# Kernel optimization log

Hardware: AMD Instinct MI355X
Metric: run time of the kernel (lower is better)

The kernel has to match this reference:

```python
import jax, jax.numpy as jnp
import numpy as np

N_ARY = 2
H = 128
X_SIZE = 128
DEPTH = 18  # levels in complete binary tree; n = 2^DEPTH - 1 = 262143 nodes


def setup_inputs() -> dict:
    key = jax.random.key(0)
    k0, k1, k2, k3 = jax.random.split(key, 4)
    n = (N_ARY ** DEPTH - 1) // (N_ARY - 1)
    x = jax.random.normal(k0, (n, X_SIZE), jnp.float32)
    W_w = jax.random.normal(k1, (2 * H, X_SIZE), jnp.float32) * 0.05
    W_b = jnp.zeros((2 * H,), jnp.float32)
    U_f = jax.random.normal(k2, (H, N_ARY * H), jnp.float32) * 0.05
    U_hc = jax.random.normal(k3, (H, N_ARY * H), jnp.float32) * 0.05
    return {"x": x, "W_w": W_w, "W_b": W_b, "U_f": U_f, "U_hc": U_hc, "depth": DEPTH}


def reference(x, W_w, W_b, U_f, U_hc, depth):
    """Tree-structured single-forget-gate MGU on a complete N_ARY tree.

    Node i (level-order) has children N_ARY*i+1 .. N_ARY*i+N_ARY. Levels are
    processed bottom-up (leaves first), matching DGL topological prop_nodes.
    """
    n_ary, h_size = N_ARY, H
    n = x.shape[0]
    wx = x @ W_w.T + W_b                      # [n, 2h]
    w_hc_x = wx[:, :h_size]                   # candidate pre-activation part
    w_f_x = wx[:, h_size:]                    # forget-gate pre-activation part
    h = jnp.zeros((n, h_size), x.dtype)
    for lvl in range(depth - 1, -1, -1):
        start = (n_ary ** lvl - 1) // (n_ary - 1)
        size = n_ary ** lvl
        whc = w_hc_x[start:start + size]
        wf = w_f_x[start:start + size]
        if lvl == depth - 1:
            # leaves: mailbox empty -> f_in = 0, h_cat = 0, h_sum = 0
            f = jax.nn.sigmoid(wf)
            new_h = (1.0 - f) * jnp.tanh(whc)
        else:
            # children of [start, start+size) occupy the contiguous next-level block
            child_start = n_ary * start + 1
            h_child = h[child_start:child_start + size * n_ary]
            h_child = h_child.reshape(size, n_ary, h_size)
            h_cat = h_child.reshape(size, n_ary * h_size)
            f = jax.nn.sigmoid(h_cat @ U_f.T + wf)
            f_rep = jnp.tile(f, (1, n_ary))
            h_cand = jnp.tanh(whc + (f_rep * h_cat) @ U_hc.T)
            new_h = f * h_child.sum(axis=1) + (1.0 - f) * h_cand
        h = h.at[start:start + size].set(new_h)
    return h
```

## Files before the change

kernel.cpp:

```cpp
#include <hip/hip_runtime.h>
#include <cmath>

#define NT 256

#define NTOT   262143
#define NINT   131071

#define WHC_OFF   0
#define WF_OFF    (NINT * 128)
#define UFT_OFF   (2 * NINT * 128)
#define UHCT_OFF  (UFT_OFF + 32768)
#define PKWW_OFF  (UHCT_OFF + 32768)
#define PKUF_OFF  (PKWW_OFF + 98304)
#define PKUHC_OFF (PKUF_OFF + 98304)
#define WS_FLOATS (PKUHC_OFF + 98304)
#define WS_BYTES  ((size_t)WS_FLOATS * 4)

#define PA_PACK 0x120100
#define PB_PACK 0x102010

typedef __attribute__((ext_vector_type(8))) short short8v;
typedef __attribute__((ext_vector_type(4))) float f32x4;

__device__ __forceinline__ float sigmoid_(float v) {
    return 1.0f / (1.0f + expf(-v));
}

__device__ __forceinline__ void split3(float a, unsigned &t0, unsigned &t1, unsigned &t2) {
    unsigned u0 = __float_as_uint(a) & 0xffff0000u;
    float f0 = __uint_as_float(u0);
    float r1 = a - f0;
    unsigned u1 = __float_as_uint(r1) & 0xffff0000u;
    float f1 = __uint_as_float(u1);
    float r2 = r1 - f1;
    unsigned u2 = __float_as_uint(r2) & 0xffff0000u;
    t0 = u0 >> 16; t1 = u1 >> 16; t2 = u2 >> 16;
}

__global__ __launch_bounds__(NT) void prep_pack(
    const float* __restrict__ Ww, const float* __restrict__ Uf,
    const float* __restrict__ Uhc, float* __restrict__ ws)
{
    int t = blockIdx.x * NT + threadIdx.x;
    if (t < 32768) { int k = t >> 7, j = t & 127; ws[UFT_OFF + t] = Uf[j * 256 + k]; return; }
    t -= 32768;
    if (t < 32768) { int k = t >> 7, j = t & 127; ws[UHCT_OFF + t] = Uhc[j * 256 + k]; return; }
    t -= 32768;

    const float* src; int term; uint4* dst; int q;
    if (t < 24576) {
        q = t;
        int l = q & 63, j = (q >> 6) & 15, s = q >> 10;
        int p = s >> 2, ks = s & 3;
        term = (PB_PACK >> (p * 4)) & 3;
        int kb = ks * 32 + (l >> 4) * 8, col = j * 16 + (l & 15);
        src = Ww + col * 128 + kb;
        dst = (uint4*)(ws + PKWW_OFF);
    } else if (t < 49152) {
        q = t - 24576;
        int l = q & 63, j = (q >> 6) & 7, s = q >> 9;
        int p = s >> 3, ks = s & 7;
        term = (PB_PACK >> (p * 4)) & 3;
        int kb = ks * 32 + (l >> 4) * 8, col = j * 16 + (l & 15);
        src = Uf + col * 256 + kb;
        dst = (uint4*)(ws + PKUF_OFF);
    } else if (t < 73728) {
        q = t - 49152;
        int l = q & 63, j = (q >> 6) & 7, s = q >> 9;
        int p = s >> 3, ks = s & 7;
        term = (PB_PACK >> (p * 4)) & 3;
        int kb = ks * 32 + (l >> 4) * 8, col = j * 16 + (l & 15);
        src = Uhc + col * 256 + kb;
        dst = (uint4*)(ws + PKUHC_OFF);
    } else return;

    unsigned hv[8];
#pragma unroll
    for (int e = 0; e < 8; ++e) {
        unsigned a, b, c; split3(src[e], a, b, c);
        hv[e] = (term == 0) ? a : (term == 1 ? b : c);
    }
    uint4 o;
    o.x = hv[0] | (hv[1] << 16); o.y = hv[2] | (hv[3] << 16);
    o.z = hv[4] | (hv[5] << 16); o.w = hv[6] | (hv[7] << 16);
    dst[q] = o;
}

#define LOADC(srcbase) { const uint4* s_ = (srcbase); \
    nx0 = s_[tid]; nx1 = s_[tid + 512]; nx2 = s_[tid + 1024]; nx3 = s_[tid + 1536]; }
#define WRITEC(dstbase) { uint4* d_ = (dstbase); \
    d_[tid] = nx0; d_[tid + 512] = nx1; d_[tid + 1024] = nx2; d_[tid + 1536] = nx3; }

__global__ __launch_bounds__(512) void wx_mfma4(
    const float* __restrict__ x, const float* __restrict__ ws_all,
    const float* __restrict__ Wb, float* __restrict__ ws, float* __restrict__ h)
{
    __shared__ short As[128 * 384];
    __shared__ uint4 sBb[2][2048];
    char* Asb = (char*)As;
    const int tid = threadIdx.x;
    const int nbase = blockIdx.x * 128;
    const uint4* pkb = (const uint4*)(ws_all + PKWW_OFF);

    uint4 nx0, nx1, nx2, nx3;
    LOADC(pkb);

    for (int i = 0; i < 8; ++i) {
        int idx = i * 512 + tid;
        int m = idx >> 5, g = idx & 31;
        int node = nbase + m; if (node > NTOT - 1) node = NTOT - 1;
        float4 v = *(const float4*)(x + (size_t)node * 128 + g * 4);
        unsigned a0[4], a1[4], a2[4];
        split3(v.x, a0[0], a1[0], a2[0]); split3(v.y, a0[1], a1[1], a2[1]);
        split3(v.z, a0[2], a1[2], a2[2]); split3(v.w, a0[3], a1[3], a2[3]);
        int ks = g >> 3, kg = (g >> 1) & 3, hw = (g & 1) * 8;
        int kss = ks ^ ((m >> 2) & 3), kgs = kg ^ (m & 3);
        char* base = Asb + m * 768 + kgs * 16 + hw;
        *(uint2*)(base + ((0 * 4 + kss) << 6)) = make_uint2(a0[0] | (a0[1] << 16), a0[2] | (a0[3] << 16));
        *(uint2*)(base + ((1 * 4 + kss) << 6)) = make_uint2(a1[0] | (a1[1] << 16), a1[2] | (a1[3] << 16));
        *(uint2*)(base + ((2 * 4 + kss) << 6)) = make_uint2(a2[0] | (a2[1] << 16), a2[2] | (a2[3] << 16));
    }
    WRITEC(&sBb[0][0]);
    __syncthreads();

    const int lane = tid & 63, wv = tid >> 6;
    const int li = lane & 15, kg = lane >> 4;
    const int mf = wv * 16 + li;
    const int mswz = (mf >> 2) & 3;
    const char* arbase = Asb + mf * 768 + ((kg ^ (mf & 3)) << 4);

    f32x4 acc[16];
#pragma unroll
    for (int j = 0; j < 16; ++j) acc[j] = (f32x4){0.f, 0.f, 0.f, 0.f};

    int cur = 0;
#pragma unroll 1
    for (int c = 0; c < 12; ++c) {
        if (c < 11) LOADC(pkb + (c + 1) * 2048);
        const int p = c >> 1, hh = c & 1;
        const int spA = (PA_PACK >> (p * 4)) & 3;
        const short8v* sBs = (const short8v*)&sBb[cur][0];
#pragma unroll
        for (int ks2 = 0; ks2 < 2; ++ks2) {
            int ks = hh * 2 + ks2;
            short8v a = *(const short8v*)(arbase + ((spA * 4 + (ks ^ mswz)) << 6));
#pragma unroll
            for (int j = 0; j < 16; ++j)
                acc[j] = __builtin_amdgcn_mfma_f32_16x16x32_bf16(a, sBs[(ks2 * 16 + j) * 64 + lane], acc[j], 0, 0, 0);
        }
        if (c < 11) WRITEC(&sBb[cur ^ 1][0]);
        __syncthreads();
        cur ^= 1;
    }

    float* whcw = ws + WHC_OFF;
    float* wfw  = ws + WF_OFF;
    const int rbase = wv * 16 + kg * 4;
#pragma unroll
    for (int r = 0; r < 4; ++r) {
        int node = nbase + rbase + r;
        if (node >= NTOT) continue;
        if (node < NINT) {
#pragma unroll
            for (int j = 0; j < 16; ++j) {
                int col = j * 16 + li;
                float v = acc[j][r] + Wb[col];
                if (col < 128) whcw[(size_t)node * 128 + col] = v;
                else           wfw [(size_t)node * 128 + col - 128] = v;
            }
        } else {
#pragma unroll
            for (int j = 0; j < 8; ++j) {
                int col = j * 16 + li;
                float hc = acc[j][r] + Wb[col];
                float wf = acc[j + 8][r] + Wb[col + 128];
                float f = sigmoid_(wf);
                h[(size_t)node * 128 + col] = (1.0f - f) * tanhf(hc);
            }
        }
    }
}


#define CHOFF(C) ((size_t)((((C) % 6) * 8 + ((C) / 6) * 4)) * 512)

#define CONVF(HLF, FS) { \
    _Pragma("unroll") \
    for (int ksl = 0; ksl < 4; ++ksl) { \
        const float* hp = h + (size_t)(2 * (s0 + rowp) + 1 + (HLF)) * 128 + kg * 8 + ksl * 32; \
        float4 va = *(const float4*)hp; \
        float4 vb = *(const float4*)(hp + 4); \
        if (FS) { \
            int fb = ksl * 32 + kg * 8; \
            float4 f0 = *(const float4*)&f_lds[rowp * 128 + (fb ^ fsw)]; \
            float4 f1 = *(const float4*)&f_lds[rowp * 128 + ((fb + 4) ^ fsw)]; \
            va.x *= f0.x; va.y *= f0.y; va.z *= f0.z; va.w *= f0.w; \
            vb.x *= f1.x; vb.y *= f1.y; vb.z *= f1.z; vb.w *= f1.w; \
        } \
        float ev[8] = {va.x, va.y, va.z, va.w, vb.x, vb.y, vb.z, vb.w}; \
        short8v t0, t1, t2; \
        _Pragma("unroll") \
        for (int e2 = 0; e2 < 8; ++e2) { \
            unsigned b0, b1, b2; split3(ev[e2], b0, b1, b2); \
            t0[e2] = (short)b0; t1[e2] = (short)b1; t2[e2] = (short)b2; \
        } \
        fr0[ksl] = t0; fr1[ksl] = t1; fr2[ksl] = t2; \
    } }

#define MFMAC(BUFP) { \
    const short8v* sBs = (const short8v*)(BUFP); \
    const int spA_ = (PA_PACK >> ((c % 6) * 4)) & 3; \
    _Pragma("unroll") \
    for (int ksl = 0; ksl < 4; ++ksl) { \
        short8v a = (spA_ == 0) ? fr0[ksl] : ((spA_ == 1) ? fr1[ksl] : fr2[ksl]); \
        _Pragma("unroll") \
        for (int jj = 0; jj < 4; ++jj) \
            acc[jj] = __builtin_amdgcn_mfma_f32_16x16x32_bf16(a, sBs[(ksl * 8 + jh * 4 + jj) * 64 + lane], acc[jj], 0, 0, 0); \
    } }

__global__ __launch_bounds__(512, 4) void lvl_reg(
    const float* __restrict__ ws_all, float* __restrict__ h, int start)
{
    __shared__ uint4 sBb[2][2048];
    float* f_lds = (float*)&sBb[0][0];
    const int tid = threadIdx.x;
    const int s0 = start + blockIdx.x * 64;
    const uint4* ufpk  = (const uint4*)(ws_all + PKUF_OFF);
    const uint4* uhcpk = (const uint4*)(ws_all + PKUHC_OFF);
    const float* wfw   = ws_all + WF_OFF;
    const float* whcw  = ws_all + WHC_OFF;

    const int lane = tid & 63, wv = tid >> 6;
    const int li = lane & 15, kg = lane >> 4;
    const int rt = wv & 3, jh = wv >> 2;
    const int rowp = rt * 16 + li;
    const int fsw = (rowp & 7) << 2;
    const int rbase = rt * 16 + kg * 4;

    short8v fr0[4], fr1[4], fr2[4];
    f32x4 acc[4];
    uint4 nx0, nx1, nx2, nx3;

#pragma unroll
    for (int j = 0; j < 4; ++j) acc[j] = (f32x4){0.f, 0.f, 0.f, 0.f};
    CONVF(0, false);
    LOADC(ufpk + CHOFF(0));
    WRITEC(&sBb[0][0]);
    __syncthreads();
    int cur = 0;
#pragma unroll 1
    for (int c = 0; c < 12; ++c) {
        if (c < 11) LOADC(ufpk + CHOFF(c + 1));
        MFMAC(&sBb[cur][0]);
        if (c == 5) CONVF(1, false);
        if (c < 11) WRITEC(&sBb[cur ^ 1][0]);
        __syncthreads();
        cur ^= 1;
    }
#pragma unroll
    for (int jj = 0; jj < 4; ++jj)
#pragma unroll
        for (int r = 0; r < 4; ++r) {
            int col = (jh * 4 + jj) * 16 + li;
            int rowl = rbase + r;
            size_t gn = (size_t)(s0 + rowl);
            float f = sigmoid_(acc[jj][r] + wfw[gn * 128 + col]);
            f_lds[rowl * 128 + (col ^ ((rowl & 7) << 2))] = f;
        }
    __syncthreads();

#pragma unroll
    for (int j = 0; j < 4; ++j) acc[j] = (f32x4){0.f, 0.f, 0.f, 0.f};
    CONVF(0, true);
    LOADC(uhcpk + CHOFF(0));
#pragma unroll 1
    for (int c = 0; c < 12; ++c) {
        WRITEC(&sBb[1][0]);
        if (c < 11) LOADC(uhcpk + CHOFF(c + 1));
        __syncthreads();
        MFMAC(&sBb[1][0]);
        if (c == 5) CONVF(1, true);
        __syncthreads();
    }

#pragma unroll
    for (int jj = 0; jj < 4; ++jj)
#pragma unroll
        for (int r = 0; r < 4; ++r) {
            int col = (jh * 4 + jj) * 16 + li;
            int rowl = rbase + r;
            size_t gn = (size_t)(s0 + rowl);
            float f = f_lds[rowl * 128 + (col ^ ((rowl & 7) << 2))];
            float whcv = whcw[gn * 128 + col];
            float c1 = h[(2 * gn + 1) * 128 + col];
            float c2 = h[(2 * gn + 2) * 128 + col];
            float t = tanhf(acc[jj][r] + whcv);
            h[gn * 128 + col] = f * (c1 + c2) + (1.0f - f) * t;
        }
}

#define B_NB 32
__global__ __launch_bounds__(NT) void level_kernel(
    const float* __restrict__ ws_all, float* __restrict__ h,
    int start, int size)
{
    __shared__ float sH[B_NB * 256];
    const float* uft  = ws_all + UFT_OFF;
    const float* uhct = ws_all + UHCT_OFF;
    const float* whcw = ws_all + WHC_OFF;
    const float* wfw  = ws_all + WF_OFF;

    const int tid = threadIdx.x;
    const int nbase = blockIdx.x * B_NB;
    const int s0 = start + nbase;
    const int nb = min(B_NB, size - nbase);

    const int jq = tid & 31;  const int j0 = jq << 2;
    const int iq = tid >> 5;  const int i0 = iq << 2;

    {
        const float4* hg = (const float4*)(h + ((size_t)2 * s0 + 1) * 128);
        float4* sH4 = (float4*)sH;
        for (int idx = tid; idx < nb * 64; idx += NT) sH4[idx] = hg[idx];
    }
    __syncthreads();

    const float4* sH4 = (const float4*)sH;

    float fv[4][4];
#pragma unroll
    for (int j = 0; j < 4; ++j)
#pragma unroll
        for (int i = 0; i < 4; ++i) fv[j][i] = 0.f;

    for (int k0 = 0; k0 < 256; k0 += 8) {
        float4 w[8];
#pragma unroll
        for (int u = 0; u < 8; ++u)
            w[u] = *(const float4*)&uft[(size_t)(k0 + u) * 128 + j0];
        float4 a[4][2];
#pragma unroll
        for (int i = 0; i < 4; ++i) {
            a[i][0] = sH4[(i0 + i) * 64 + (k0 >> 2)];
            a[i][1] = sH4[(i0 + i) * 64 + (k0 >> 2) + 1];
        }
#pragma unroll
        for (int u = 0; u < 8; ++u) {
            const float* wp = (const float*)&w[u];
#pragma unroll
            for (int i = 0; i < 4; ++i) {
                float av = ((const float*)&a[i][u >> 2])[u & 3];
#pragma unroll
                for (int j = 0; j < 4; ++j)
                    fv[j][i] = fmaf(wp[j], av, fv[j][i]);
            }
        }
    }
#pragma unroll
    for (int i = 0; i < 4; ++i) {
        float4 wfv = *(const float4*)&wfw[(size_t)(s0 + i0 + i) * 128 + j0];
        const float* wfp = (const float*)&wfv;
#pragma unroll
        for (int j = 0; j < 4; ++j)
            fv[j][i] = sigmoid_(fv[j][i] + wfp[j]);
    }

    __syncthreads();

    float hs[4][4];
#pragma unroll
    for (int i = 0; i < 4; ++i) {
        float4* row = (float4*)&sH[(i0 + i) * 256];
        float4 c0 = row[jq];
        float4 c1 = row[32 + jq];
        hs[0][i] = c0.x + c1.x;
        hs[1][i] = c0.y + c1.y;
        hs[2][i] = c0.z + c1.z;
        hs[3][i] = c0.w + c1.w;
        c0.x *= fv[0][i]; c0.y *= fv[1][i]; c0.z *= fv[2][i]; c0.w *= fv[3][i];
        c1.x *= fv[0][i]; c1.y *= fv[1][i]; c1.z *= fv[2][i]; c1.w *= fv[3][i];
        row[jq] = c0;
        row[32 + jq] = c1;
    }
    __syncthreads();

    float cv[4][4];
#pragma unroll
    for (int j = 0; j < 4; ++j)
#pragma unroll
        for (int i = 0; i < 4; ++i) cv[j][i] = 0.f;

    for (int k0 = 0; k0 < 256; k0 += 8) {
        float4 w[8];
#pragma unroll
        for (int u = 0; u < 8; ++u)
            w[u] = *(const float4*)&uhct[(size_t)(k0 + u) * 128 + j0];
        float4 a[4][2];
#pragma unroll
        for (int i = 0; i < 4; ++i) {
            a[i][0] = sH4[(i0 + i) * 64 + (k0 >> 2)];
            a[i][1] = sH4[(i0 + i) * 64 + (k0 >> 2) + 1];
        }
#pragma unroll
        for (int u = 0; u < 8; ++u) {
            const float* wp = (const float*)&w[u];
#pragma unroll
            for (int i = 0; i < 4; ++i) {
                float av = ((const float*)&a[i][u >> 2])[u & 3];
#pragma unroll
                for (int j = 0; j < 4; ++j)
                    cv[j][i] = fmaf(wp[j], av, cv[j][i]);
            }
        }
    }

#pragma unroll
    for (int i = 0; i < 4; ++i) {
        if (i0 + i < nb) {
            float4 whcv = *(const float4*)&whcw[(size_t)(s0 + i0 + i) * 128 + j0];
            const float* wp = (const float*)&whcv;
            float4 o;
            float* op = (float*)&o;
#pragma unroll
            for (int j = 0; j < 4; ++j) {
                float t = tanhf(cv[j][i] + wp[j]);
                op[j] = fv[j][i] * hs[j][i] + (1.0f - fv[j][i]) * t;
            }
            *(float4*)&h[(size_t)(s0 + i0 + i) * 128 + j0] = o;
        }
    }
}

__global__ __launch_bounds__(NT) void tail_kernel(
    const float* __restrict__ ws_all, float* __restrict__ h)
{
    __shared__ __align__(16) float bufA[64 * 128];
    __shared__ __align__(16) float bufB[32 * 128];
    __shared__ __align__(16) float sF[8 * 128];
    const float* uft  = ws_all + UFT_OFF;
    const float* uhct = ws_all + UHCT_OFF;
    const float* whcw = ws_all + WHC_OFF;
    const float* wfw  = ws_all + WF_OFF;

    const int tid = threadIdx.x;
    const int jq = tid & 31;  const int j0 = jq << 2;
    const int iq = tid >> 5;

    {
        const float4* hg = (const float4*)(h + (size_t)63 * 128);
        float4* b4 = (float4*)bufA;
        for (int idx = tid; idx < 64 * 32; idx += NT) b4[idx] = hg[idx];
    }
    __syncthreads();

    float* child = bufA;
    float* cur   = bufB;

    for (int lvl = 5; lvl >= 0; --lvl) {
        const int start = (1 << lvl) - 1;
        const int size  = 1 << lvl;
        for (int pass = 0; pass < size; pass += 8) {
            const int ni = pass + iq;
            const bool act = (ni < size);
            float f[4] = {0.f, 0.f, 0.f, 0.f};
            if (act) {
                const float* hc = child + ni * 256;
                float fv[4] = {0.f, 0.f, 0.f, 0.f};
                for (int k = 0; k < 256; k += 4) {
#pragma unroll
                    for (int u = 0; u < 4; ++u) {
                        float av = hc[k + u];
                        float4 w = *(const float4*)&uft[(size_t)(k + u) * 128 + j0];
                        fv[0] = fmaf(w.x, av, fv[0]);
                        fv[1] = fmaf(w.y, av, fv[1]);
                        fv[2] = fmaf(w.z, av, fv[2]);
                        fv[3] = fmaf(w.w, av, fv[3]);
                    }
                }
                const int gn = start + ni;
                float4 wfv = *(const float4*)&wfw[(size_t)gn * 128 + j0];
                const float* wfp = (const float*)&wfv;
#pragma unroll
                for (int j = 0; j < 4; ++j) {
                    f[j] = sigmoid_(fv[j] + wfp[j]);
                    sF[iq * 128 + j0 + j] = f[j];
                }
            }
            __syncthreads();
            if (act) {
                const float* hc = child + ni * 256;
                const float* fr = sF + iq * 128;
                float cv[4] = {0.f, 0.f, 0.f, 0.f};
                for (int k = 0; k < 256; k += 4) {
#pragma unroll
                    for (int u = 0; u < 4; ++u) {
                        float av = hc[k + u] * fr[(k + u) & 127];
                        float4 w = *(const float4*)&uhct[(size_t)(k + u) * 128 + j0];
                        cv[0] = fmaf(w.x, av, cv[0]);
                        cv[1] = fmaf(w.y, av, cv[1]);
                        cv[2] = fmaf(w.z, av, cv[2]);
                        cv[3] = fmaf(w.w, av, cv[3]);
                    }
                }
                const int gn = start + ni;
                float4 whcv = *(const float4*)&whcw[(size_t)gn * 128 + j0];
                const float* wp = (const float*)&whcv;
                float4 o;
                float* op = (float*)&o;
#pragma unroll
                for (int j = 0; j < 4; ++j) {
                    float hsum = hc[j0 + j] + hc[128 + j0 + j];
                    float t = tanhf(cv[j] + wp[j]);
                    op[j] = f[j] * hsum + (1.0f - f[j]) * t;
                }
                *(float4*)&cur[ni * 128 + j0] = o;
                *(float4*)&h[(size_t)gn * 128 + j0] = o;
            }
            __syncthreads();
        }
        float* t = child; child = cur; cur = t;
    }
}


__global__ __launch_bounds__(NT) void fb_leaf(
    const float* __restrict__ x, const float* __restrict__ Ww,
    const float* __restrict__ Wb, float* __restrict__ h, int start, int size)
{
    __shared__ float sA[32 * 128];
    __shared__ float sW[16 * 260];
    const int tid = threadIdx.x;
    const int nbase = blockIdx.x * 32;
    const int s0 = start + nbase;
    const int nb = min(32, size - nbase);
    const int jq = tid & 31, iq = tid >> 5;
    const int j0 = jq << 2, i0 = iq << 2;
    {
        const float4* xg = (const float4*)(x + (size_t)s0 * 128);
        float4* sA4 = (float4*)sA;
        for (int idx = tid; idx < nb * 32; idx += NT) sA4[idx] = xg[idx];
    }
    float whc[4][4], wf[4][4];
#pragma unroll
    for (int j = 0; j < 4; ++j)
#pragma unroll
        for (int i = 0; i < 4; ++i) { whc[j][i] = 0.f; wf[j][i] = 0.f; }
    for (int k0 = 0; k0 < 128; k0 += 16) {
        __syncthreads();
        const float4* Wg = (const float4*)Ww;
        for (int idx = tid; idx < 256 * 4; idx += NT) {
            int j2 = idx >> 2, kq = idx & 3;
            float4 v = Wg[j2 * 32 + (k0 >> 2) + kq];
            int kb = kq << 2;
            sW[(kb + 0) * 260 + j2] = v.x; sW[(kb + 1) * 260 + j2] = v.y;
            sW[(kb + 2) * 260 + j2] = v.z; sW[(kb + 3) * 260 + j2] = v.w;
        }
        __syncthreads();
#pragma unroll
        for (int kk = 0; kk < 16; kk += 4) {
            float4 a4[4];
#pragma unroll
            for (int i = 0; i < 4; ++i)
                a4[i] = ((const float4*)sA)[(i0 + i) * 32 + ((k0 + kk) >> 2)];
#pragma unroll
            for (int u = 0; u < 4; ++u) {
                int k = kk + u;
                float4 w0 = *((const float4*)&sW[k * 260 + j0]);
                float4 w1 = *((const float4*)&sW[k * 260 + 128 + j0]);
                const float* w0p = (const float*)&w0;
                const float* w1p = (const float*)&w1;
#pragma unroll
                for (int i = 0; i < 4; ++i) {
                    float av = ((const float*)&a4[i])[u];
#pragma unroll
                    for (int j = 0; j < 4; ++j) {
                        whc[j][i] = fmaf(w0p[j], av, whc[j][i]);
                        wf[j][i]  = fmaf(w1p[j], av, wf[j][i]);
                    }
                }
            }
        }
    }
#pragma unroll
    for (int i = 0; i < 4; ++i) {
        if (i0 + i < nb) {
            float4 o; float* op = (float*)&o;
#pragma unroll
            for (int j = 0; j < 4; ++j) {
                float f = sigmoid_(wf[j][i] + Wb[128 + j0 + j]);
                op[j] = (1.0f - f) * tanhf(whc[j][i] + Wb[j0 + j]);
            }
            *(float4*)&h[((size_t)(s0 + i0 + i)) * 128 + j0] = o;
        }
    }
}

__global__ __launch_bounds__(NT) void fb_internal(
    const float* __restrict__ x, const float* __restrict__ Ww,
    const float* __restrict__ Wb, const float* __restrict__ Uf,
    const float* __restrict__ Uhc, float* __restrict__ h, int start, int size)
{
    __shared__ float sA[32 * 256];
    __shared__ float sW[4224];
    const int tid = threadIdx.x;
    const int nbase = blockIdx.x * 32;
    const int s0 = start + nbase;
    const int nb = min(32, size - nbase);
    const int jq = tid & 31, iq = tid >> 5;
    const int j0 = jq << 2, i0 = iq << 2;
    {
        const float4* xg = (const float4*)(x + (size_t)s0 * 128);
        float4* sA4 = (float4*)sA;
        for (int idx = tid; idx < nb * 32; idx += NT) sA4[idx] = xg[idx];
    }
    float whc[4][4], wf[4][4];
#pragma unroll
    for (int j = 0; j < 4; ++j)
#pragma unroll
        for (int i = 0; i < 4; ++i) { whc[j][i] = 0.f; wf[j][i] = 0.f; }
    for (int k0 = 0; k0 < 128; k0 += 16) {
        __syncthreads();
        const float4* Wg = (const float4*)Ww;
        for (int idx = tid; idx < 256 * 4; idx += NT) {
            int j2 = idx >> 2, kq = idx & 3;
            float4 v = Wg[j2 * 32 + (k0 >> 2) + kq];
            int kb = kq << 2;
            sW[(kb + 0) * 260 + j2] = v.x; sW[(kb + 1) * 260 + j2] = v.y;
            sW[(kb + 2) * 260 + j2] = v.z; sW[(kb + 3) * 260 + j2] = v.w;
        }
        __syncthreads();
#pragma unroll
        for (int kk = 0; kk < 16; kk += 4) {
            float4 a4[4];
#pragma unroll
            for (int i = 0; i < 4; ++i)
                a4[i] = ((const float4*)sA)[(i0 + i) * 32 + ((k0 + kk) >> 2)];
#pragma unroll
            for (int u = 0; u < 4; ++u) {
                int k = kk + u;
                float4 w0 = *((const float4*)&sW[k * 260 + j0]);
                float4 w1 = *((const float4*)&sW[k * 260 + 128 + j0]);
                const float* w0p = (const float*)&w0;
                const float* w1p = (const float*)&w1;
#pragma unroll
                for (int i = 0; i < 4; ++i) {
                    float av = ((const float*)&a4[i])[u];
#pragma unroll
                    for (int j = 0; j < 4; ++j) {
                        whc[j][i] = fmaf(w0p[j], av, whc[j][i]);
                        wf[j][i]  = fmaf(w1p[j], av, wf[j][i]);
                    }
                }
            }
        }
    }
#pragma unroll
    for (int j = 0; j < 4; ++j) {
        float bhc = Wb[j0 + j], bf = Wb[128 + j0 + j];
#pragma unroll
        for (int i = 0; i < 4; ++i) { whc[j][i] += bhc; wf[j][i] += bf; }
    }
    __syncthreads();
    {
        const float4* hg = (const float4*)(h + ((size_t)2 * s0 + 1) * 128);
        float4* sA4 = (float4*)sA;
        for (int idx = tid; idx < nb * 64; idx += NT) sA4[idx] = hg[idx];
    }
    float fv[4][4];
#pragma unroll
    for (int j = 0; j < 4; ++j)
#pragma unroll
        for (int i = 0; i < 4; ++i) fv[j][i] = 0.f;
    for (int k0 = 0; k0 < 256; k0 += 32) {
        __syncthreads();
        const float4* Ug = (const float4*)Uf;
        for (int idx = tid; idx < 128 * 8; idx += NT) {
            int j2 = idx >> 3, kq = idx & 7;
            float4 v = Ug[j2 * 64 + (k0 >> 2) + kq];
            int kb = kq << 2;
            sW[(kb + 0) * 132 + j2] = v.x; sW[(kb + 1) * 132 + j2] = v.y;
            sW[(kb + 2) * 132 + j2] = v.z; sW[(kb + 3) * 132 + j2] = v.w;
        }
        __syncthreads();
#pragma unroll
        for (int kk = 0; kk < 32; kk += 4) {
            float4 a4[4];
#pragma unroll
            for (int i = 0; i < 4; ++i)
                a4[i] = ((const float4*)sA)[(i0 + i) * 64 + ((k0 + kk) >> 2)];
#pragma unroll
            for (int u = 0; u < 4; ++u) {
                int k = kk + u;
                float4 w = *((const float4*)&sW[k * 132 + j0]);
                const float* wp = (const float*)&w;
#pragma unroll
                for (int i = 0; i < 4; ++i) {
                    float av = ((const float*)&a4[i])[u];
#pragma unroll
                    for (int j = 0; j < 4; ++j)
                        fv[j][i] = fmaf(wp[j], av, fv[j][i]);
                }
            }
        }
    }
#pragma unroll
    for (int j = 0; j < 4; ++j)
#pragma unroll
        for (int i = 0; i < 4; ++i)
            fv[j][i] = sigmoid_(fv[j][i] + wf[j][i]);
    __syncthreads();
    float hs[4][4];
#pragma unroll
    for (int i = 0; i < 4; ++i) {
        float4* row = (float4*)&sA[(i0 + i) * 256];
        float4 c0 = row[jq], c1 = row[32 + jq];
        hs[0][i] = c0.x + c1.x; hs[1][i] = c0.y + c1.y;
        hs[2][i] = c0.z + c1.z; hs[3][i] = c0.w + c1.w;
        c0.x *= fv[0][i]; c0.y *= fv[1][i]; c0.z *= fv[2][i]; c0.w *= fv[3][i];
        c1.x *= fv[0][i]; c1.y *= fv[1][i]; c1.z *= fv[2][i]; c1.w *= fv[3][i];
        row[jq] = c0; row[32 + jq] = c1;
    }
    float cv[4][4];
#pragma unroll
    for (int j = 0; j < 4; ++j)
#pragma unroll
        for (int i = 0; i < 4; ++i) cv[j][i] = 0.f;
    for (int k0 = 0; k0 < 256; k0 += 32) {
        __syncthreads();
        const float4* Ug = (const float4*)Uhc;
        for (int idx = tid; idx < 128 * 8; idx += NT) {
            int j2 = idx >> 3, kq = idx & 7;
            float4 v = Ug[j2 * 64 + (k0 >> 2) + kq];
            int kb = kq << 2;
            sW[(kb + 0) * 132 + j2] = v.x; sW[(kb + 1) * 132 + j2] = v.y;
            sW[(kb + 2) * 132 + j2] = v.z; sW[(kb + 3) * 132 + j2] = v.w;
        }
        __syncthreads();
#pragma unroll
        for (int kk = 0; kk < 32; kk += 4) {
            float4 a4[4];
#pragma unroll
            for (int i = 0; i < 4; ++i)
                a4[i] = ((const float4*)sA)[(i0 + i) * 64 + ((k0 + kk) >> 2)];
#pragma unroll
            for (int u = 0; u < 4; ++u) {
                int k = kk + u;
                float4 w = *((const float4*)&sW[k * 132 + j0]);
                const float* wp = (const float*)&w;
#pragma unroll
                for (int i = 0; i < 4; ++i) {
                    float av = ((const float*)&a4[i])[u];
#pragma unroll
                    for (int j = 0; j < 4; ++j)
                        cv[j][i] = fmaf(wp[j], av, cv[j][i]);
                }
            }
        }
    }
#pragma unroll
    for (int i = 0; i < 4; ++i) {
        if (i0 + i < nb) {
            float4 o; float* op = (float*)&o;
#pragma unroll
            for (int j = 0; j < 4; ++j) {
                float t = tanhf(cv[j][i] + whc[j][i]);
                op[j] = fv[j][i] * hs[j][i] + (1.0f - fv[j][i]) * t;
            }
            *(float4*)&h[((size_t)(s0 + i0 + i)) * 128 + j0] = o;
        }
    }
}


extern "C" void kernel_launch(void* const* d_in, const int* in_sizes, int n_in,
                              void* d_out, int out_size, void* d_ws, size_t ws_size,
                              hipStream_t stream)
{
    (void)in_sizes; (void)n_in; (void)out_size;
    const float* x   = (const float*)d_in[0];
    const float* Ww  = (const float*)d_in[1];
    const float* Wb  = (const float*)d_in[2];
    const float* Uf  = (const float*)d_in[3];
    const float* Uhc = (const float*)d_in[4];
    float* h = (float*)d_out;
    const int depth = 18;

    if (ws_size >= WS_BYTES) {
        float* ws = (float*)d_ws;
        prep_pack<<<544, NT, 0, stream>>>(Ww, Uf, Uhc, ws);
        wx_mfma4<<<2048, 512, 0, stream>>>(x, ws, Wb, ws, h);
        for (int lvl = 16; lvl >= 12; --lvl)
            lvl_reg<<<1 << (lvl - 6), 512, 0, stream>>>(ws, h, (1 << lvl) - 1);
        for (int lvl = 11; lvl >= 6; --lvl) {
            int start = (1 << lvl) - 1;
            int size  = 1 << lvl;
            level_kernel<<<(size + B_NB - 1) / B_NB, NT, 0, stream>>>(ws, h, start, size);
        }
        tail_kernel<<<1, NT, 0, stream>>>(ws, h);
    } else {
        {
            int lvl = depth - 1;
            int start = (1 << lvl) - 1, size = 1 << lvl;
            fb_leaf<<<(size + 31) / 32, NT, 0, stream>>>(x, Ww, Wb, h, start, size);
        }
        for (int lvl = depth - 2; lvl >= 0; --lvl) {
            int start = (1 << lvl) - 1, size = 1 << lvl;
            fb_internal<<<(size + 31) / 32, NT, 0, stream>>>(x, Ww, Wb, Uf, Uhc, h, start, size);
        }
    }
}
```

Measured before the change: 799.8 us.

## Keep x bf16 split fragments in registers and halve rows per block in wx GEMM

Result: slower. 961.4 us (+20.2%).

```diff
diff --git a/kernel.cpp b/kernel.cpp
--- a/kernel.cpp
+++ b/kernel.cpp
@@ -91,62 +91,63 @@
 #define WRITEC(dstbase) { uint4* d_ = (dstbase); \
     d_[tid] = nx0; d_[tid + 512] = nx1; d_[tid + 1024] = nx2; d_[tid + 1536] = nx3; }
 
-__global__ __launch_bounds__(512) void wx_mfma4(
+__global__ __launch_bounds__(512, 4) void wx_reg(
     const float* __restrict__ x, const float* __restrict__ ws_all,
     const float* __restrict__ Wb, float* __restrict__ ws, float* __restrict__ h)
 {
-    __shared__ short As[128 * 384];
     __shared__ uint4 sBb[2][2048];
-    char* Asb = (char*)As;
     const int tid = threadIdx.x;
-    const int nbase = blockIdx.x * 128;
+    const int nbase = blockIdx.x * 64;
     const uint4* pkb = (const uint4*)(ws_all + PKWW_OFF);
+
+    const int lane = tid & 63, wv = tid >> 6;
+    const int li = lane & 15, kg = lane >> 4;
+    const int rt = wv & 3, jh = wv >> 2;
+    const int rowp = rt * 16 + li;
+
+    short8v fr0[4], fr1[4], fr2[4];
+    {
+        int node = nbase + rowp; if (node > NTOT - 1) node = NTOT - 1;
+        const float* xrow = x + (size_t)node * 128 + kg * 8;
+#pragma unroll
+        for (int ksl = 0; ksl < 4; ++ksl) {
+            float4 va = *(const float4*)(xrow + ksl * 32);
+            float4 vb = *(const float4*)(xrow + ksl * 32 + 4);
+            float ev[8] = {va.x, va.y, va.z, va.w, vb.x, vb.y, vb.z, vb.w};
+            short8v t0, t1, t2;
+#pragma unroll
+            for (int e = 0; e < 8; ++e) {
+                unsigned b0, b1, b2; split3(ev[e], b0, b1, b2);
+                t0[e] = (short)b0; t1[e] = (short)b1; t2[e] = (short)b2;
+            }
+            fr0[ksl] = t0; fr1[ksl] = t1; fr2[ksl] = t2;
+        }
+    }
 
     uint4 nx0, nx1, nx2, nx3;
     LOADC(pkb);
-
-    for (int i = 0; i < 8; ++i) {
-        int idx = i * 512 + tid;
-        int m = idx >> 5, g = idx & 31;
-        int node = nbase + m; if (node > NTOT - 1) node = NTOT - 1;
-        float4 v = *(const float4*)(x + (size_t)node * 128 + g * 4);
-        unsigned a0[4], a1[4], a2[4];
-        split3(v.x, a0[0], a1[0], a2[0]); split3(v.y, a0[1], a1[1], a2[1]);
-        split3(v.z, a0[2], a1[2], a2[2]); split3(v.w, a0[3], a1[3], a2[3]);
-        int ks = g >> 3, kg = (g >> 1) & 3, hw = (g & 1) * 8;
-        int kss = ks ^ ((m >> 2) & 3), kgs = kg ^ (m & 3);
-        char* base = Asb + m * 768 + kgs * 16 + hw;
-        *(uint2*)(base + ((0 * 4 + kss) << 6)) = make_uint2(a0[0] | (a0[1] << 16), a0[2] | (a0[3] << 16));
-        *(uint2*)(base + ((1 * 4 + kss) << 6)) = make_uint2(a1[0] | (a1[1] << 16), a1[2] | (a1[3] << 16));
-        *(uint2*)(base + ((2 * 4 + kss) << 6)) = make_uint2(a2[0] | (a2[1] << 16), a2[2] | (a2[3] << 16));
-    }
     WRITEC(&sBb[0][0]);
     __syncthreads();
 
-    const int lane = tid & 63, wv = tid >> 6;
-    const int li = lane & 15, kg = lane >> 4;
-    const int mf = wv * 16 + li;
-    const int mswz = (mf >> 2) & 3;
-    const char* arbase = Asb + mf * 768 + ((kg ^ (mf & 3)) << 4);
-
-    f32x4 acc[16];
-#pragma unroll
-    for (int j = 0; j < 16; ++j) acc[j] = (f32x4){0.f, 0.f, 0.f, 0.f};
+    f32x4 acc[8];
+#pragma unroll
+    for (int j = 0; j < 8; ++j) acc[j] = (f32x4){0.f, 0.f, 0.f, 0.f};
 
     int cur = 0;
 #pragma unroll 1
     for (int c = 0; c < 12; ++c) {
-        if (c < 11) LOADC(pkb + (c + 1) * 2048);
-        const int p = c >> 1, hh = c & 1;
-        const int spA = (PA_PACK >> (p * 4)) & 3;
+        if (c < 11) LOADC(pkb + (size_t)(c + 1) * 2048);
         const short8v* sBs = (const short8v*)&sBb[cur][0];
 #pragma unroll
-        for (int ks2 = 0; ks2 < 2; ++ks2) {
-            int ks = hh * 2 + ks2;
-            short8v a = *(const short8v*)(arbase + ((spA * 4 + (ks ^ mswz)) << 6));
-#pragma unroll
-            for (int j = 0; j < 16; ++j)
-                acc[j] = __builtin_amdgcn_mfma_f32_16x16x32_bf16(a, sBs[(ks2 * 16 + j) * 64 + lane], acc[j], 0, 0, 0);
+        for (int u = 0; u < 2; ++u) {
+            int s = 2 * c + u;
+            int p = s >> 2, ksl = s & 3;
+            int spA = (PA_PACK >> (p * 4)) & 3;
+            short8v a = (spA == 0) ? fr0[ksl] : ((spA == 1) ? fr1[ksl] : fr2[ksl]);
+#pragma unroll
+            for (int jj = 0; jj < 8; ++jj)
+                acc[jj] = __builtin_amdgcn_mfma_f32_16x16x32_bf16(
+                    a, sBs[u * 1024 + (jh * 8 + jj) * 64 + lane], acc[jj], 0, 0, 0);
         }
         if (c < 11) WRITEC(&sBb[cur ^ 1][0]);
         __syncthreads();
@@ -155,32 +156,50 @@
 
     float* whcw = ws + WHC_OFF;
     float* wfw  = ws + WF_OFF;
-    const int rbase = wv * 16 + kg * 4;
+    float* sF = (float*)&sBb[0][0];
+    const int rbase0 = rt * 16 + kg * 4;
+    if (jh == 1) {
+#pragma unroll
+        for (int jj = 0; jj < 8; ++jj) {
+            int colr = jj * 16 + li;
+            float bia = Wb[128 + colr];
+#pragma unroll
+            for (int r = 0; r < 4; ++r)
+                sF[(rbase0 + r) * 128 + colr] = acc[jj][r] + bia;
+        }
+    }
+    __syncthreads();
+
 #pragma unroll
     for (int r = 0; r < 4; ++r) {
-        int node = nbase + rbase + r;
+        int row = rbase0 + r;
+        int node = nbase + row;
         if (node >= NTOT) continue;
         if (node < NINT) {
-#pragma unroll
-            for (int j = 0; j < 16; ++j) {
-                int col = j * 16 + li;
-                float v = acc[j][r] + Wb[col];
-                if (col < 128) whcw[(size_t)node * 128 + col] = v;
-                else           wfw [(size_t)node * 128 + col - 128] = v;
-            }
-        } else {
-#pragma unroll
-            for (int j = 0; j < 8; ++j) {
-                int col = j * 16 + li;
-                float hc = acc[j][r] + Wb[col];
-                float wf = acc[j + 8][r] + Wb[col + 128];
-                float f = sigmoid_(wf);
+            if (jh == 0) {
+#pragma unroll
+                for (int jj = 0; jj < 8; ++jj) {
+                    int col = jj * 16 + li;
+                    whcw[(size_t)node * 128 + col] = acc[jj][r] + Wb[col];
+                }
+            } else {
+#pragma unroll
+                for (int jj = 0; jj < 8; ++jj) {
+                    int col = jj * 16 + li;
+                    wfw[(size_t)node * 128 + col] = acc[jj][r] + Wb[128 + col];
+                }
+            }
+        } else if (jh == 0) {
+#pragma unroll
+            for (int jj = 0; jj < 8; ++jj) {
+                int col = jj * 16 + li;
+                float hc = acc[jj][r] + Wb[col];
+                float f = sigmoid_(sF[row * 128 + col]);
                 h[(size_t)node * 128 + col] = (1.0f - f) * tanhf(hc);
             }
         }
     }
 }
-
 
 #define CHOFF(C) ((size_t)((((C) % 6) * 8 + ((C) / 6) * 4)) * 512)
 
@@ -788,7 +807,7 @@
     if (ws_size >= WS_BYTES) {
         float* ws = (float*)d_ws;
         prep_pack<<<544, NT, 0, stream>>>(Ww, Uf, Uhc, ws);
-        wx_mfma4<<<2048, 512, 0, stream>>>(x, ws, Wb, ws, h);
+        wx_reg<<<(NTOT + 63) / 64, 512, 0, stream>>>(x, ws, Wb, ws, h);
         for (int lvl = 16; lvl >= 12; --lvl)
             lvl_reg<<<1 << (lvl - 6), 512, 0, stream>>>(ws, h, (1 << lvl) - 1);
         for (int lvl = 11; lvl >= 6; --lvl) {
```
